# Kernel tuning notes

Measured on AMD Instinct MI355X. Metric: run time of the kernel, lower is better.

Reference implementation:

```python
import jax, jax.numpy as jnp
import numpy as np

N = 65536   # batch_size * timeseries
D = 512     # feature dim of h_real
K = 64      # n_clusters


def setup_inputs() -> dict:
    key = jax.random.key(0)
    k1, k2 = jax.random.split(key)
    h_real = jax.random.normal(k1, (N, D), dtype=jnp.float32)
    # F is an (approximately) orthogonal projection parameter [N, K].
    F = jax.random.normal(k2, (N, K), dtype=jnp.float32)
    return {"h_real": h_real, "F": F}


def reference(h_real, F):
    # Original: WTW = h h^T (N x N); loss = trace(WTW) - trace(F^T WTW F).
    # Algebraically identical reduced form, never materializing the N x N Gram:
    #   trace(h h^T) = sum(h * h)
    #   trace(F^T h h^T F) = ||F^T h||_F^2
    tr_wtw = jnp.sum(h_real * h_real)
    G = F.T @ h_real                      # [K, D] skinny GEMM
    tr_proj = jnp.sum(G * G)
    return tr_wtw - tr_proj
```

## Files before the change

kernel.cpp:

```cpp
#include <hip/hip_runtime.h>
#include <hip/hip_fp16.h>
#include <hip/hip_bf16.h>

#define N_TOT 65536
#define D_DIM 512
#define K_DIM 64
#define NC    32
#define GSZ   (K_DIM * D_DIM)

typedef __bf16   bf16x8 __attribute__((ext_vector_type(8)));
typedef float    f32x4  __attribute__((ext_vector_type(4)));
typedef _Float16 half8  __attribute__((ext_vector_type(8)));

union pk4 { unsigned int u[4]; bf16x8 v; };

__device__ __forceinline__ unsigned int pack2(float a, float b) {
    __hip_bfloat162 t = __float22bfloat162_rn(make_float2(a, b));
    union { __hip_bfloat162 h; unsigned int u; } r; r.h = t;
    return r.u;
}

extern "C" __global__ void __launch_bounds__(1024)
k1_partial(const float* __restrict__ h, const float* __restrict__ F,
           float* __restrict__ trw_out, unsigned short* __restrict__ gpart,
           float* __restrict__ out, int rowsPerBlock) {
    __shared__ float red[16];

    const int tid = threadIdx.x;
    const int b   = blockIdx.x;
    if (b == 0 && tid == 0) out[0] = 0.0f;

    const int wave = tid >> 6;
    const int lane = tid & 63;
    const int m    = lane & 15;
    const int q    = lane >> 4;

    const int row0    = b * rowsPerBlock;
    const int nChunks = rowsPerBlock / NC;

    f32x4 acc[4][2];
    #pragma unroll
    for (int kt = 0; kt < 4; ++kt)
        #pragma unroll
        for (int dt = 0; dt < 2; ++dt)
            acc[kt][dt] = (f32x4){0.f, 0.f, 0.f, 0.f};

    float trw = 0.f;

    const float* hb = h + (size_t)(row0 + q * 8) * D_DIM + wave * 32 + m;
    const float* fb = F + (size_t)(row0 + q * 8) * K_DIM + m;

    for (int c = 0; c < nChunks; ++c) {
        float vb[16], va[32];
        #pragma unroll
        for (int dt = 0; dt < 2; ++dt)
            #pragma unroll
            for (int j = 0; j < 8; ++j)
                vb[dt * 8 + j] = hb[(size_t)j * D_DIM + dt * 16];
        #pragma unroll
        for (int kk = 0; kk < 4; ++kk)
            #pragma unroll
            for (int j = 0; j < 8; ++j)
                va[kk * 8 + j] = fb[(size_t)j * K_DIM + kk * 16];

        bf16x8 bfrag[2], afrag[4];
        #pragma unroll
        for (int dt = 0; dt < 2; ++dt) {
            pk4 p;
            #pragma unroll
            for (int jj = 0; jj < 4; ++jj) {
                float a0 = vb[dt * 8 + 2 * jj], a1 = vb[dt * 8 + 2 * jj + 1];
                trw += a0 * a0 + a1 * a1;
                p.u[jj] = pack2(a0, a1);
            }
            bfrag[dt] = p.v;
        }
        #pragma unroll
        for (int kk = 0; kk < 4; ++kk) {
            pk4 p;
            #pragma unroll
            for (int jj = 0; jj < 4; ++jj)
                p.u[jj] = pack2(va[kk * 8 + 2 * jj], va[kk * 8 + 2 * jj + 1]);
            afrag[kk] = p.v;
        }

        #pragma unroll
        for (int kt = 0; kt < 4; ++kt)
            #pragma unroll
            for (int dt = 0; dt < 2; ++dt)
                acc[kt][dt] = __builtin_amdgcn_mfma_f32_16x16x32_bf16(
                    afrag[kt], bfrag[dt], acc[kt][dt], 0, 0, 0);

        hb += (size_t)NC * D_DIM;
        fb += (size_t)NC * K_DIM;
    }

    {
        const int bn2 = (b + 1) & 255;
        const float* hb2 = h + (size_t)(bn2 * rowsPerBlock + q * 8) * D_DIM
                             + wave * 32 + m;
        float trw2 = 0.f;
        for (int c = 0; c < nChunks; ++c) {
            float v2[16];
            #pragma unroll
            for (int dt = 0; dt < 2; ++dt)
                #pragma unroll
                for (int j = 0; j < 8; ++j)
                    v2[dt * 8 + j] = hb2[(size_t)j * D_DIM + dt * 16];
            #pragma unroll
            for (int i = 0; i < 16; ++i) trw2 += v2[i] * v2[i];
            hb2 += (size_t)NC * D_DIM;
        }
        union { float f; unsigned int u; } tw; tw.f = trw2;
        if ((tw.u ^ 0xAAAAAAAAu) == 0x12345u)
            trw += trw2;
    }

    unsigned short* gp = gpart + (size_t)b * GSZ;
    #pragma unroll
    for (int kt = 0; kt < 4; ++kt)
        #pragma unroll
        for (int dt = 0; dt < 2; ++dt)
            #pragma unroll
            for (int r = 0; r < 4; ++r) {
                const int k = kt * 16 + q * 4 + r;
                const int d = wave * 32 + dt * 16 + m;
                __half hv = __float2half(acc[kt][dt][r]);
                gp[k * D_DIM + d] = *(unsigned short*)&hv;
            }

    #pragma unroll
    for (int off = 32; off > 0; off >>= 1) trw += __shfl_down(trw, off, 64);
    if (lane == 0) red[wave] = trw;
    __syncthreads();
    if (tid == 0) {
        float s = 0.f;
        #pragma unroll
        for (int w = 0; w < 16; ++w) s += red[w];
        trw_out[b] = s;
    }
}

extern "C" __global__ void __launch_bounds__(512)
k2_reduce(const float* __restrict__ trw, const unsigned short* __restrict__ gpart,
          float* __restrict__ out, int P) {
    __shared__ float sh[32 * 16 * 8];
    __shared__ float red2[8];

    const int tid = threadIdx.x;
    const int sub = tid >> 4;
    const int oct = tid & 15;
    const int tt  = blockIdx.x * 16 + oct;

    float g[8];
    #pragma unroll
    for (int j = 0; j < 8; ++j) g[j] = 0.f;

    const unsigned short* base = gpart + (size_t)tt * 8;
    for (int b = sub; b < P; b += 32) {
        half8 v = *(const half8*)(base + (size_t)b * GSZ);
        #pragma unroll
        for (int j = 0; j < 8; ++j) g[j] += (float)v[j];
    }
    #pragma unroll
    for (int j = 0; j < 8; ++j) sh[(sub * 16 + oct) * 8 + j] = g[j];
    __syncthreads();

    float val = 0.f;
    if (tid < 128) {
        const int o2 = tid >> 3, j = tid & 7;
        float s = 0.f;
        #pragma unroll
        for (int sb = 0; sb < 32; ++sb) s += sh[(sb * 16 + o2) * 8 + j];
        val = -s * s;
    } else if (blockIdx.x == 0 && tid - 128 < P) {
        val = trw[tid - 128];
    }

    #pragma unroll
    for (int off = 32; off > 0; off >>= 1) val += __shfl_down(val, off, 64);
    if ((tid & 63) == 0) red2[tid >> 6] = val;
    __syncthreads();
    if (tid == 0) {
        float s = 0.f;
        #pragma unroll
        for (int w = 0; w < 8; ++w) s += red2[w];
        atomicAdd(out, s);
    }
}

extern "C" void kernel_launch(void* const* d_in, const int* in_sizes, int n_in,
                              void* d_out, int out_size, void* d_ws, size_t ws_size,
                              hipStream_t stream) {
    const float* h = (const float*)d_in[0];
    const float* F = (const float*)d_in[1];
    float* out = (float*)d_out;

    int P = 256;
    while (P > 1 && (size_t)4096 + (size_t)P * (GSZ * 2) > ws_size) P >>= 1;
    const int rowsPerBlock = N_TOT / P;

    float* trw = (float*)d_ws;
    unsigned short* gpart = (unsigned short*)((char*)d_ws + 4096);

    hipLaunchKernelGGL(k1_partial, dim3(P), dim3(1024), 0, stream,
                       h, F, trw, gpart, out, rowsPerBlock);
    hipLaunchKernelGGL(k2_reduce, dim3(256), dim3(512), 0, stream,
                       trw, gpart, out, P);
}
```

Measured before the change: 222.6 us.

## Double-buffer h/F chunks into LDS via async global-to-LDS loads; drop redundant pass

```diff
diff --git a/kernel.cpp b/kernel.cpp
--- a/kernel.cpp
+++ b/kernel.cpp
@@ -20,10 +20,19 @@
     return r.u;
 }
 
+typedef __attribute__((address_space(3))) void       lds_void;
+typedef __attribute__((address_space(1))) const void gbl_void;
+
+__device__ __forceinline__ void dma16(const float* g, float* l) {
+    __builtin_amdgcn_global_load_lds((gbl_void*)g, (lds_void*)l, 16, 0, 0);
+}
+
 extern "C" __global__ void __launch_bounds__(1024)
 k1_partial(const float* __restrict__ h, const float* __restrict__ F,
            float* __restrict__ trw_out, unsigned short* __restrict__ gpart,
            float* __restrict__ out, int rowsPerBlock) {
+    __shared__ float hbuf[2][NC][D_DIM];
+    __shared__ float fbuf[2][NC][K_DIM];
     __shared__ float red[16];
 
     const int tid = threadIdx.x;
@@ -47,41 +56,51 @@
 
     float trw = 0.f;
 
-    const float* hb = h + (size_t)(row0 + q * 8) * D_DIM + wave * 32 + m;
-    const float* fb = F + (size_t)(row0 + q * 8) * K_DIM + m;
+    auto stage = [&](int c, int p) {
+        const int r0 = row0 + c * NC;
+        const float* g = h + (size_t)(r0 + 2 * wave) * D_DIM + lane * 4;
+        #pragma unroll
+        for (int rr = 0; rr < 2; ++rr)
+            #pragma unroll
+            for (int hf = 0; hf < 2; ++hf)
+                dma16(g + rr * D_DIM + hf * 256, &hbuf[p][2 * wave + rr][hf * 256]);
+        if (wave < 8) {
+            const float* gf = F + (size_t)(r0 + 4 * wave) * K_DIM + lane * 4;
+            dma16(gf, &fbuf[p][4 * wave][0]);
+        }
+    };
+
+    stage(0, 0);
 
     for (int c = 0; c < nChunks; ++c) {
-        float vb[16], va[32];
-        #pragma unroll
-        for (int dt = 0; dt < 2; ++dt)
+        __syncthreads();
+        if (c + 1 < nChunks) stage(c + 1, (c + 1) & 1);
+
+        const int p = c & 1;
+        bf16x8 bfrag[2], afrag[4];
+        #pragma unroll
+        for (int dt = 0; dt < 2; ++dt) {
+            float v[8];
+            #pragma unroll
+            for (int j = 0; j < 8; ++j) {
+                v[j] = hbuf[p][q * 8 + j][wave * 32 + dt * 16 + m];
+                trw += v[j] * v[j];
+            }
+            pk4 pp;
+            #pragma unroll
+            for (int jj = 0; jj < 4; ++jj) pp.u[jj] = pack2(v[2*jj], v[2*jj+1]);
+            bfrag[dt] = pp.v;
+        }
+        #pragma unroll
+        for (int kt = 0; kt < 4; ++kt) {
+            float v[8];
             #pragma unroll
             for (int j = 0; j < 8; ++j)
-                vb[dt * 8 + j] = hb[(size_t)j * D_DIM + dt * 16];
-        #pragma unroll
-        for (int kk = 0; kk < 4; ++kk)
-            #pragma unroll
-            for (int j = 0; j < 8; ++j)
-                va[kk * 8 + j] = fb[(size_t)j * K_DIM + kk * 16];
-
-        bf16x8 bfrag[2], afrag[4];
-        #pragma unroll
-        for (int dt = 0; dt < 2; ++dt) {
-            pk4 p;
-            #pragma unroll
-            for (int jj = 0; jj < 4; ++jj) {
-                float a0 = vb[dt * 8 + 2 * jj], a1 = vb[dt * 8 + 2 * jj + 1];
-                trw += a0 * a0 + a1 * a1;
-                p.u[jj] = pack2(a0, a1);
-            }
-            bfrag[dt] = p.v;
-        }
-        #pragma unroll
-        for (int kk = 0; kk < 4; ++kk) {
-            pk4 p;
-            #pragma unroll
-            for (int jj = 0; jj < 4; ++jj)
-                p.u[jj] = pack2(va[kk * 8 + 2 * jj], va[kk * 8 + 2 * jj + 1]);
-            afrag[kk] = p.v;
+                v[j] = fbuf[p][q * 8 + j][kt * 16 + m];
+            pk4 pp;
+            #pragma unroll
+            for (int jj = 0; jj < 4; ++jj) pp.u[jj] = pack2(v[2*jj], v[2*jj+1]);
+            afrag[kt] = pp.v;
         }
 
         #pragma unroll
@@ -90,30 +109,6 @@
             for (int dt = 0; dt < 2; ++dt)
                 acc[kt][dt] = __builtin_amdgcn_mfma_f32_16x16x32_bf16(
                     afrag[kt], bfrag[dt], acc[kt][dt], 0, 0, 0);
-
-        hb += (size_t)NC * D_DIM;
-        fb += (size_t)NC * K_DIM;
-    }
-
-    {
-        const int bn2 = (b + 1) & 255;
-        const float* hb2 = h + (size_t)(bn2 * rowsPerBlock + q * 8) * D_DIM
-                             + wave * 32 + m;
-        float trw2 = 0.f;
-        for (int c = 0; c < nChunks; ++c) {
-            float v2[16];
-            #pragma unroll
-            for (int dt = 0; dt < 2; ++dt)
-                #pragma unroll
-                for (int j = 0; j < 8; ++j)
-                    v2[dt * 8 + j] = hb2[(size_t)j * D_DIM + dt * 16];
-            #pragma unroll
-            for (int i = 0; i < 16; ++i) trw2 += v2[i] * v2[i];
-            hb2 += (size_t)NC * D_DIM;
-        }
-        union { float f; unsigned int u; } tw; tw.f = trw2;
-        if ((tw.u ^ 0xAAAAAAAAu) == 0x12345u)
-            trw += trw2;
     }
 
     unsigned short* gp = gpart + (size_t)b * GSZ;
```

New measurement: 213.5 us. 4.1% less time.
